# Optimization experiments

Measured on AMD Instinct MI355X. Metric: run time of the kernel, lower is better.

## Reference

```python
import jax, jax.numpy as jnp
import numpy as np

DN = jax.lax.conv_dimension_numbers((1, 32, 32, 32, 1), (3, 3, 3, 1, 32), ('NDHWC', 'DHWIO', 'NDHWC'))


def setup_inputs() -> dict:
    key = jax.random.key(0)
    k0, k1, k2, k3, k4 = jax.random.split(key, 5)
    B = 64
    x = jax.random.normal(k0, (B, 32, 32, 32, 1), dtype=jnp.float32)
    # conv weights in DHWIO layout; kaiming-ish scale
    w1 = jax.random.normal(k1, (3, 3, 3, 1, 32), dtype=jnp.float32) * (1.0 / np.sqrt(27 * 1))
    b1 = jax.random.normal(k2, (32,), dtype=jnp.float32) * 0.01
    w2 = jax.random.normal(k3, (3, 3, 3, 32, 64), dtype=jnp.float32) * (1.0 / np.sqrt(27 * 32))
    b2 = jax.random.normal(k4, (64,), dtype=jnp.float32) * 0.01
    return {"x": x, "w1": w1, "b1": b1, "w2": w2, "b2": b2}


def _conv3d_valid(x, w):
    # x: [B, D, H, W, C_in], w: [kD, kH, kW, C_in, C_out] -> [B, D-2, H-2, W-2, C_out]
    dn = jax.lax.conv_dimension_numbers(x.shape, w.shape, ('NDHWC', 'DHWIO', 'NDHWC'))
    return jax.lax.conv_general_dilated(x, w, window_strides=(1, 1, 1),
                                        padding='VALID', dimension_numbers=dn)


def reference(x, w1, b1, w2, b2):
    # Dense input -> all voxels active, so spconv's gather-GEMM-scatter equals
    # a dense valid 3D conv. ReLU acts on active-site features == dense ReLU.
    h = jax.nn.relu(_conv3d_valid(x, w1) + b1)        # [B, 30, 30, 30, 32]
    h = jax.nn.relu(_conv3d_valid(h, w2) + b2)        # [B, 28, 28, 28, 64]
    # spconv ToDense returns NCDHW
    return jnp.transpose(h, (0, 4, 1, 2, 3))          # [B, 64, 28, 28, 28]
```

## Files before the change

### kernel.cpp

```cpp
#include <hip/hip_runtime.h>
#include <cstdint>
#include <cstddef>

typedef __attribute__((ext_vector_type(8))) short bf16x8;
typedef __attribute__((ext_vector_type(4))) float f32x4;
typedef __attribute__((ext_vector_type(4))) unsigned int u32x4;
typedef unsigned short u16;

#define H1_ROW_B   1920
#define H1_BATCH   (30 * 30 * 960)
#define LDS_STRIDE 1952
#define OUT_CSTR   21952

__device__ __forceinline__ u16 f2bf(float f) {
    union { float f; unsigned u; } v; v.f = f;
    unsigned r = v.u + 0x7FFF + ((v.u >> 16) & 1);
    return (u16)(r >> 16);
}

__device__ __forceinline__ void fma4(float4& a, float s, const float4& w) {
    a.x = fmaf(s, w.x, a.x);
    a.y = fmaf(s, w.y, a.y);
    a.z = fmaf(s, w.z, a.z);
    a.w = fmaf(s, w.w, a.w);
}

__global__ __launch_bounds__(256) void conv1_relu(
    const float* __restrict__ x, const float* __restrict__ w1,
    const float* __restrict__ b1, u16* __restrict__ h1, int b0)
{
    __shared__ float wl[27 * 32 + 32];

    const int z   = blockIdx.x;
    const int yt  = blockIdx.y;
    const int bl  = blockIdx.z;
    const int b   = b0 + bl;
    const int tid = threadIdx.x;

    for (int i = tid; i < 27 * 32; i += 256) wl[i] = w1[i];
    if (tid < 32) wl[27 * 32 + tid] = b1[tid];
    __syncthreads();

    const int c4   = tid & 7;
    const int slot = tid >> 3;

    const float4 bias = *reinterpret_cast<const float4*>(&wl[27 * 32 + c4 * 4]);
    const float* xb  = x + (size_t)b * 32768;
    u16*         h1b = h1 + (size_t)bl * H1_BATCH;

    if (slot < 30) {
#pragma unroll 1
        for (int j = 0; j < 3; ++j) {
            const int p  = slot + 30 * j;
            const int yy = p / 15;
            const int xx = (p - yy * 15) * 2;
            const int y  = yt * 6 + yy;

            float4 acc0 = bias, acc1 = bias;
#pragma unroll
            for (int kd = 0; kd < 3; ++kd) {
#pragma unroll
                for (int kh = 0; kh < 3; ++kh) {
                    const float* row = xb + ((size_t)(z + kd) * 32 + (y + kh)) * 32 + xx;
                    const float2 v01 = *reinterpret_cast<const float2*>(row);
                    const float2 v23 = *reinterpret_cast<const float2*>(row + 2);
                    const int t = (kd * 3 + kh) * 3;
                    const float4 w0  = *reinterpret_cast<const float4*>(&wl[(t + 0) * 32 + c4 * 4]);
                    const float4 w1v = *reinterpret_cast<const float4*>(&wl[(t + 1) * 32 + c4 * 4]);
                    const float4 w2v = *reinterpret_cast<const float4*>(&wl[(t + 2) * 32 + c4 * 4]);
                    fma4(acc0, v01.x, w0);
                    fma4(acc0, v01.y, w1v);
                    fma4(acc0, v23.x, w2v);
                    fma4(acc1, v01.y, w0);
                    fma4(acc1, v23.x, w1v);
                    fma4(acc1, v23.y, w2v);
                }
            }
            ushort4 s0, s1;
            s0.x = f2bf(fmaxf(acc0.x, 0.f)); s0.y = f2bf(fmaxf(acc0.y, 0.f));
            s0.z = f2bf(fmaxf(acc0.z, 0.f)); s0.w = f2bf(fmaxf(acc0.w, 0.f));
            s1.x = f2bf(fmaxf(acc1.x, 0.f)); s1.y = f2bf(fmaxf(acc1.y, 0.f));
            s1.z = f2bf(fmaxf(acc1.z, 0.f)); s1.w = f2bf(fmaxf(acc1.w, 0.f));
            u16* dst = h1b + ((size_t)(z * 30 + y) * 30 + xx) * 32 + c4 * 4;
            *reinterpret_cast<ushort4*>(dst)      = s0;
            *reinterpret_cast<ushort4*>(dst + 32) = s1;
        }
    }
}

__global__ __launch_bounds__(256) void pack_w2(
    const float* __restrict__ w2, u16* __restrict__ wB)
{
    const int tap = blockIdx.x;
    const int tid = threadIdx.x;
    const int nt = tid >> 6;
    const int l  = tid & 63;
    const int r = l & 15, q = l >> 4;
    u16* dst = wB + ((size_t)(tap * 4 + nt) * 64 + l) * 8;
#pragma unroll
    for (int j = 0; j < 8; ++j)
        dst[j] = f2bf(w2[(size_t)(tap * 32 + q * 8 + j) * 64 + nt * 16 + r]);
}

template<int NMT, int XOUT>
__device__ __forceinline__ void conv2_body(
    const unsigned char* smem, const char* wBl,
    const float* __restrict__ b2, float* __restrict__ out,
    int b, int y0, int z0, int zw, int l)
{
    const int r = l & 15, q = l >> 4;
    const int yl = r >> 2, xg = r & 3;

    f32x4 acc[NMT][4];
#pragma unroll
    for (int nt = 0; nt < 4; ++nt) {
        const float bv = b2[nt * 16 + r];
        const f32x4 bi = {bv, bv, bv, bv};
#pragma unroll
        for (int mt = 0; mt < NMT; ++mt) acc[mt][nt] = bi;
    }

    const unsigned char* aBase =
        smem + (zw * 6 + yl) * LDS_STRIDE + (XOUT + xg) * 64 + q * 16;

    u32x4 Bs[2][4];
#define B_LOAD(slot, t)                                                        \
    { const char* p_ = wBl + (size_t)(t) * 4096;                               \
      asm volatile("global_load_dwordx4 %0, %4, off\n\t"                       \
                   "global_load_dwordx4 %1, %4, off offset:1024\n\t"           \
                   "global_load_dwordx4 %2, %4, off offset:2048\n\t"           \
                   "global_load_dwordx4 %3, %4, off offset:3072"               \
                   : "=&v"(Bs[slot][0]), "=&v"(Bs[slot][1]),                   \
                     "=&v"(Bs[slot][2]), "=&v"(Bs[slot][3])                    \
                   : "v"(p_)); }

    B_LOAD(0, 0)

#pragma unroll
    for (int tap = 0; tap < 27; ++tap) {
        const int cur = tap & 1;

        if (tap < 26) B_LOAD(cur ^ 1, tap + 1)

        if (tap < 26) asm volatile("s_waitcnt vmcnt(4)");
        else          asm volatile("s_waitcnt vmcnt(0)");

        asm volatile("" : "+v"(Bs[cur][0]), "+v"(Bs[cur][1]),
                          "+v"(Bs[cur][2]), "+v"(Bs[cur][3]));
        const bf16x8 B0 = __builtin_bit_cast(bf16x8, Bs[cur][0]);
        const bf16x8 B1 = __builtin_bit_cast(bf16x8, Bs[cur][1]);
        const bf16x8 B2 = __builtin_bit_cast(bf16x8, Bs[cur][2]);
        const bf16x8 B3 = __builtin_bit_cast(bf16x8, Bs[cur][3]);

        const int kd = tap / 9;
        const int kh = (tap - kd * 9) / 3;
        const int kw = tap - kd * 9 - kh * 3;
        const unsigned char* ap = aBase + (kd * 6 + kh) * LDS_STRIDE + kw * 64;

        __builtin_amdgcn_s_setprio(1);
#pragma unroll
        for (int mt = 0; mt < NMT; ++mt) {
            const bf16x8 a = *reinterpret_cast<const bf16x8*>(ap + mt * 256);
            acc[mt][0] = __builtin_amdgcn_mfma_f32_16x16x32_bf16(a, B0, acc[mt][0], 0, 0, 0);
            acc[mt][1] = __builtin_amdgcn_mfma_f32_16x16x32_bf16(a, B1, acc[mt][1], 0, 0, 0);
            acc[mt][2] = __builtin_amdgcn_mfma_f32_16x16x32_bf16(a, B2, acc[mt][2], 0, 0, 0);
            acc[mt][3] = __builtin_amdgcn_mfma_f32_16x16x32_bf16(a, B3, acc[mt][3], 0, 0, 0);
        }
        __builtin_amdgcn_s_setprio(0);
    }
#undef B_LOAD

    const int z = z0 + zw;
    float* ob = out + ((size_t)b * 64 + r) * OUT_CSTR
                    + (size_t)z * 784 + (size_t)(y0 + q) * 28 + XOUT;
#pragma unroll
    for (int mt = 0; mt < NMT; ++mt) {
#pragma unroll
        for (int nt = 0; nt < 4; ++nt) {
            const f32x4 v = acc[mt][nt];
            float4 st;
            st.x = fmaxf(v.x, 0.f);
            st.y = fmaxf(v.y, 0.f);
            st.z = fmaxf(v.z, 0.f);
            st.w = fmaxf(v.w, 0.f);
            *reinterpret_cast<float4*>(ob + (size_t)nt * 16 * OUT_CSTR + mt * 4) = st;
        }
    }
}

__global__ __launch_bounds__(512, 4) void conv2_mfma(
    const u16* __restrict__ h1, const u16* __restrict__ wB,
    const float* __restrict__ b2, float* __restrict__ out, int b0)
{
    __shared__ __align__(16) unsigned char smem[36 * LDS_STRIDE];

    const int g   = gridDim.x;
    const int bid = blockIdx.x;
    const int lb  = (g % 8 == 0) ? ((bid & 7) * (g >> 3) + (bid >> 3)) : bid;

    const int t0  = lb % 49;
    const int bl  = lb / 49;
    const int yg  = t0 % 7;
    const int zt  = t0 / 7;

    const int b  = b0 + bl;
    const int y0 = yg * 4, z0 = zt * 4;
    const int tid = threadIdx.x;
    const int wv  = tid >> 6;
    const int l   = tid & 63;
    const int zw  = wv >> 1;
    const int xh  = wv & 1;

    const char* wBl = (const char*)wB + l * 16;

    {
        const char* gbase = (const char*)(h1 + (size_t)bl * H1_BATCH);
        for (int c = wv; c < 72; c += 8) {
            const int rid = c >> 1, half = c & 1;
            const int zz = rid / 6, yy = rid - zz * 6;
            const char* src = gbase
                + (size_t)((z0 + zz) * 30 + (y0 + yy)) * H1_ROW_B
                + half * 896 + l * 16;
            unsigned char* dst = smem + rid * LDS_STRIDE + half * 896 + l * 16;
            __builtin_amdgcn_global_load_lds(
                (const __attribute__((address_space(1))) void*)src,
                (__attribute__((address_space(3))) void*)dst, 16, 0, 0);
        }
    }
    __syncthreads();

    if (xh == 0)
        conv2_body<4, 0>(smem, wBl, b2, out, b, y0, z0, zw, l);
    else
        conv2_body<3, 16>(smem, wBl, b2, out, b, y0, z0, zw, l);
}

extern "C" void kernel_launch(void* const* d_in, const int* in_sizes, int n_in,
                              void* d_out, int out_size, void* d_ws, size_t ws_size,
                              hipStream_t stream)
{
    const float* x  = (const float*)d_in[0];
    const float* w1 = (const float*)d_in[1];
    const float* b1 = (const float*)d_in[2];
    const float* w2 = (const float*)d_in[3];
    const float* b2 = (const float*)d_in[4];
    float* out = (float*)d_out;

    u16* wB = (u16*)d_ws;
    u16* h1 = (u16*)((char*)d_ws + 131072);

    pack_w2<<<27, 256, 0, stream>>>(w2, wB);

    const size_t per_batch = (size_t)H1_BATCH * 2;
    size_t avail = ws_size > 131072 ? ws_size - 131072 : 0;
    int bchunk = (int)(avail / per_batch);
    if (bchunk < 1)  bchunk = 1;
    if (bchunk > 64) bchunk = 64;

    for (int b0 = 0; b0 < 64; b0 += bchunk) {
        int bc = 64 - b0;
        if (bc > bchunk) bc = bchunk;
        conv1_relu<<<dim3(30, 5, bc), 256, 0, stream>>>(x, w1, b1, h1, b0);
        conv2_mfma<<<dim3(49 * bc), 512, 0, stream>>>(h1, wB, b2, out, b0);
    }
}
```

Baseline: 297.8 us.

## Stage conv2 weight taps in shared LDS double buffer instead of per-wave global loads

Each wave used to fetch every B-weight tap from global memory straight into registers, with a register double buffer. Now one wave per tap issues global_load_lds into a double-buffered 8KB LDS region, and all waves read their B fragments from LDS. A __syncthreads after every tap keeps the buffers consistent. This cuts redundant weight fetches across the 8 waves, but adds 27 block-wide barriers, extra LDS reads, and 8KB more LDS per block.

```diff
diff --git a/kernel.cpp b/kernel.cpp
--- a/kernel.cpp
+++ b/kernel.cpp
@@ -4,12 +4,12 @@
 
 typedef __attribute__((ext_vector_type(8))) short bf16x8;
 typedef __attribute__((ext_vector_type(4))) float f32x4;
-typedef __attribute__((ext_vector_type(4))) unsigned int u32x4;
 typedef unsigned short u16;
 
 #define H1_ROW_B   1920
 #define H1_BATCH   (30 * 30 * 960)
 #define LDS_STRIDE 1952
+#define B_LDS_OFF  (36 * LDS_STRIDE)
 #define OUT_CSTR   21952
 
 __device__ __forceinline__ u16 f2bf(float f) {
@@ -104,9 +104,9 @@
 
 template<int NMT, int XOUT>
 __device__ __forceinline__ void conv2_body(
-    const unsigned char* smem, const char* wBl,
+    const unsigned char* smem, const char* wBb,
     const float* __restrict__ b2, float* __restrict__ out,
-    int b, int y0, int z0, int zw, int l)
+    int b, int y0, int z0, int zw, int wv, int l)
 {
     const int r = l & 15, q = l >> 4;
     const int yl = r >> 2, xg = r & 3;
@@ -122,35 +122,26 @@
 
     const unsigned char* aBase =
         smem + (zw * 6 + yl) * LDS_STRIDE + (XOUT + xg) * 64 + q * 16;
-
-    u32x4 Bs[2][4];
-#define B_LOAD(slot, t)                                                        \
-    { const char* p_ = wBl + (size_t)(t) * 4096;                               \
-      asm volatile("global_load_dwordx4 %0, %4, off\n\t"                       \
-                   "global_load_dwordx4 %1, %4, off offset:1024\n\t"           \
-                   "global_load_dwordx4 %2, %4, off offset:2048\n\t"           \
-                   "global_load_dwordx4 %3, %4, off offset:3072"               \
-                   : "=&v"(Bs[slot][0]), "=&v"(Bs[slot][1]),                   \
-                     "=&v"(Bs[slot][2]), "=&v"(Bs[slot][3])                    \
-                   : "v"(p_)); }
-
-    B_LOAD(0, 0)
+    const unsigned char* bBase = smem + B_LDS_OFF + (size_t)l * 16;
 
 #pragma unroll
     for (int tap = 0; tap < 27; ++tap) {
-        const int cur = tap & 1;
-
-        if (tap < 26) B_LOAD(cur ^ 1, tap + 1)
-
-        if (tap < 26) asm volatile("s_waitcnt vmcnt(4)");
-        else          asm volatile("s_waitcnt vmcnt(0)");
-
-        asm volatile("" : "+v"(Bs[cur][0]), "+v"(Bs[cur][1]),
-                          "+v"(Bs[cur][2]), "+v"(Bs[cur][3]));
-        const bf16x8 B0 = __builtin_bit_cast(bf16x8, Bs[cur][0]);
-        const bf16x8 B1 = __builtin_bit_cast(bf16x8, Bs[cur][1]);
-        const bf16x8 B2 = __builtin_bit_cast(bf16x8, Bs[cur][2]);
-        const bf16x8 B3 = __builtin_bit_cast(bf16x8, Bs[cur][3]);
+        if (tap < 26 && wv == ((tap + 1) & 7)) {
+            const char* bsrc = wBb + (size_t)(tap + 1) * 4096 + l * 16;
+            unsigned char* bdst = const_cast<unsigned char*>(
+                smem) + B_LDS_OFF + ((tap + 1) & 1) * 4096 + l * 16;
+#pragma unroll
+            for (int k = 0; k < 4; ++k)
+                __builtin_amdgcn_global_load_lds(
+                    (const __attribute__((address_space(1))) void*)(bsrc + k * 1024),
+                    (__attribute__((address_space(3))) void*)(bdst + k * 1024), 16, 0, 0);
+        }
+
+        const unsigned char* bb = bBase + (tap & 1) * 4096;
+        const bf16x8 B0 = *reinterpret_cast<const bf16x8*>(bb);
+        const bf16x8 B1 = *reinterpret_cast<const bf16x8*>(bb + 1024);
+        const bf16x8 B2 = *reinterpret_cast<const bf16x8*>(bb + 2048);
+        const bf16x8 B3 = *reinterpret_cast<const bf16x8*>(bb + 3072);
 
         const int kd = tap / 9;
         const int kh = (tap - kd * 9) / 3;
@@ -167,8 +158,9 @@
             acc[mt][3] = __builtin_amdgcn_mfma_f32_16x16x32_bf16(a, B3, acc[mt][3], 0, 0, 0);
         }
         __builtin_amdgcn_s_setprio(0);
-    }
-#undef B_LOAD
+
+        __syncthreads();
+    }
 
     const int z = z0 + zw;
     float* ob = out + ((size_t)b * 64 + r) * OUT_CSTR
@@ -192,7 +184,7 @@
     const u16* __restrict__ h1, const u16* __restrict__ wB,
     const float* __restrict__ b2, float* __restrict__ out, int b0)
 {
-    __shared__ __align__(16) unsigned char smem[36 * LDS_STRIDE];
+    __shared__ __align__(16) unsigned char smem[B_LDS_OFF + 8192];
 
     const int g   = gridDim.x;
     const int bid = blockIdx.x;
@@ -211,7 +203,7 @@
     const int zw  = wv >> 1;
     const int xh  = wv & 1;
 
-    const char* wBl = (const char*)wB + l * 16;
+    const char* wBb = (const char*)wB;
 
     {
         const char* gbase = (const char*)(h1 + (size_t)bl * H1_BATCH);
@@ -227,12 +219,21 @@
                 (__attribute__((address_space(3))) void*)dst, 16, 0, 0);
         }
     }
+    if (wv == 0) {
+        const char* bsrc = wBb + l * 16;
+        unsigned char* bdst = smem + B_LDS_OFF + l * 16;
+#pragma unroll
+        for (int k = 0; k < 4; ++k)
+            __builtin_amdgcn_global_load_lds(
+                (const __attribute__((address_space(1))) void*)(bsrc + k * 1024),
+                (__attribute__((address_space(3))) void*)(bdst + k * 1024), 16, 0, 0);
+    }
     __syncthreads();
 
     if (xh == 0)
-        conv2_body<4, 0>(smem, wBl, b2, out, b, y0, z0, zw, l);
+        conv2_body<4, 0>(smem, wBb, b2, out, b, y0, z0, zw, wv, l);
     else
-        conv2_body<3, 16>(smem, wBl, b2, out, b, y0, z0, zw, l);
+        conv2_body<3, 16>(smem, wBb, b2, out, b, y0, z0, zw, wv, l);
 }
 
 extern "C" void kernel_launch(void* const* d_in, const int* in_sizes, int n_in,
```

Result: slower. 304.3 us (+2.2%).
